# Optimization experiments

Measured on AMD Instinct MI355X. Metric: run time of the kernel, lower is better.

Reference implementation:

```python
import jax, jax.numpy as jnp
import numpy as np

L, N, D, E, KD = 4, 40000, 128, 320000, 16
DECAY, N_ITER, EPS = 0.5, 3, 1e-5


def setup_inputs() -> dict:
    key = jax.random.key(0)
    ks = jax.random.split(key, 16)
    s = 0.05
    return {
        "x": jax.random.normal(ks[0], (L, N, D), jnp.float32),
        "edge_rows": jax.random.randint(ks[1], (E,), 0, N, jnp.int32),
        "edge_cols": jax.random.randint(ks[2], (E,), 0, N, jnp.int32),
        "edge_vals": jax.random.uniform(ks[3], (E,), jnp.float32) * 0.1,
        "sage_W": jax.random.normal(ks[4], (D, D), jnp.float32) * s,
        "sage_b": jnp.zeros((D,), jnp.float32),
        "sage_agg_W": jax.random.normal(ks[5], (D, D), jnp.float32) * s,
        "key_W": jax.random.normal(ks[6], (D, KD), jnp.float32) * s,
        "query_W": jax.random.normal(ks[7], (D, KD), jnp.float32) * s,
        "value_W": jax.random.normal(ks[8], (D, D), jnp.float32) * s,
        "attn_ln_g": jnp.ones((D,), jnp.float32),
        "attn_ln_b": jnp.zeros((D,), jnp.float32),
        "lin_W": jax.random.normal(ks[9], (D, D), jnp.float32) * s,
        "lin_b": jnp.zeros((D,), jnp.float32),
        "ln_g": jnp.ones((D,), jnp.float32),
        "ln_b": jnp.zeros((D,), jnp.float32),
    }


def _layernorm(x, g, b):
    mu = jnp.mean(x, axis=-1, keepdims=True)
    var = jnp.mean((x - mu) ** 2, axis=-1, keepdims=True)
    return (x - mu) * jax.lax.rsqrt(var + EPS) * g + b


def _spmm(rows, cols, vals, x2d):
    # sparse [N,N] @ dense [N,F]: out[r] = sum_e vals[e] * x2d[cols[e]] for rows[e]==r
    return jax.ops.segment_sum(vals[:, None] * x2d[cols], rows, num_segments=N)


def reference(x, edge_rows, edge_cols, edge_vals, sage_W, sage_b, sage_agg_W,
              key_W, query_W, value_W, attn_ln_g, attn_ln_b,
              lin_W, lin_b, ln_g, ln_b):
    # x: [L, N, D]
    x2d = jnp.transpose(x, (1, 0, 2)).reshape(N, L * D)  # [N, L*D]

    # ---- SAGEConv ----
    proj = x @ sage_W + sage_b
    agg = _spmm(edge_rows, edge_cols, edge_vals, x2d)
    agg = jnp.transpose(agg.reshape(N, L, D), (1, 0, 2)) @ sage_agg_W
    sage_out = jax.nn.silu(proj + agg)

    # ---- RetentiveAttention ----
    weights = jnp.mean((x @ key_W) * (x @ query_W), axis=-1, keepdims=True)
    x_acc = x
    cur = x2d
    for _ in range(1, N_ITER):
        cur = _spmm(edge_rows, edge_cols, edge_vals, cur * DECAY)
        xr = jnp.transpose(cur.reshape(N, L, D), (1, 0, 2))  # [L, N, D]
        weights = weights + jnp.mean((xr @ key_W) * (xr @ query_W), axis=-1, keepdims=True)
        x_acc = x_acc + xr
    attn_out = _layernorm((x_acc @ value_W) * weights, attn_ln_g, attn_ln_b)

    # ---- GPSConv fusion ----
    y = jax.nn.silu((sage_out + attn_out) @ lin_W + lin_b)
    return _layernorm(y, ln_g, ln_b)
```

## Files before the change

### kernel.cpp

```cpp
#include <hip/hip_runtime.h>
#include <math.h>

#define LL 4
#define NN 40000
#define DD 128
#define EE 320000
#define ROWS (LL*NN)
#define ND (NN*DD)
#define EPS_LN 1e-5f

typedef __attribute__((ext_vector_type(8))) short bf16x8;
typedef __attribute__((ext_vector_type(4))) short s16x4;
typedef __attribute__((ext_vector_type(4))) float f32x4;

#define OFF_CNT      0
#define OFF_ROWPTR   40000
#define OFF_ROWOFS   80004
#define OFF_CCOLS    120004
#define OFF_CVALS    440004
#define OFF_WBF      760004
#define OFF_A        829636
#define OFF_B        (OFF_A + ROWS*DD/2)
#define OFF_XBF      (OFF_B + ROWS*DD/2)

#define WB_W0  0
#define WB_W1  32768
#define WB_WV  65536
#define WB_WL  98304
#define WB_K   131072
#define WB_Q   135168
#define WB_LO_BIG 16384
#define WB_LO_KQ  2048
#define WB_LOGICAL 69632

__device__ __forceinline__ unsigned fu(float f) { union { float f; unsigned u; } v; v.f = f; return v.u; }
__device__ __forceinline__ float uf(unsigned u) { union { unsigned u; float f; } v; v.u = u; return v.f; }

__device__ __forceinline__ short f2bf(float f) {
    unsigned u = fu(f);
    unsigned r = u + 0x7fffu + ((u >> 16) & 1u);
    return (short)(r >> 16);
}
__device__ __forceinline__ float bf2f(short h) { return uf(((unsigned)(unsigned short)h) << 16); }
__device__ __forceinline__ void splitbf(float v, short& h, short& l) {
    h = f2bf(v);
    l = f2bf(v - bf2f(h));
}

__device__ __forceinline__ unsigned pack_hi(float a, float b) {
    return (fu(a) >> 16) | (fu(b) & 0xffff0000u);
}
__device__ __forceinline__ float resid(float a) {
    return a - uf(fu(a) & 0xffff0000u);
}

union FragU { bf16x8 v; unsigned u[4]; };

__global__ void k_hist(const int* __restrict__ rows, int* __restrict__ cnt) {
    int e = blockIdx.x * 256 + threadIdx.x;
    if (e < EE) atomicAdd(&cnt[rows[e]], 1);
}

__global__ __launch_bounds__(1024) void k_scan1(const int* __restrict__ cnt,
                                                int* __restrict__ row_ptr,
                                                int* __restrict__ bsum) {
    __shared__ int wtot[16];
    int tid = threadIdx.x, lane = tid & 63, wid = tid >> 6;
    int i = blockIdx.x * 1024 + tid;
    int v = (i < NN) ? cnt[i] : 0;
    int incl = v;
    #pragma unroll
    for (int off = 1; off < 64; off <<= 1) {
        int t = __shfl_up(incl, off);
        if (lane >= off) incl += t;
    }
    if (lane == 63) wtot[wid] = incl;
    __syncthreads();
    if (wid == 0) {
        int wv = (lane < 16) ? wtot[lane] : 0;
        #pragma unroll
        for (int off = 1; off < 16; off <<= 1) {
            int t = __shfl_up(wv, off);
            if (lane >= off) wv += t;
        }
        if (lane < 16) wtot[lane] = wv;
    }
    __syncthreads();
    int excl = ((wid > 0) ? wtot[wid - 1] : 0) + incl - v;
    if (i < NN) row_ptr[i] = excl;
    if (tid == 0) bsum[blockIdx.x] = wtot[15];
}

__global__ void k_scan2(const int* __restrict__ bsum, int* __restrict__ bofs) {
    int lane = threadIdx.x;
    int v = (lane < 40) ? bsum[lane] : 0;
    int incl = v;
    #pragma unroll
    for (int off = 1; off < 64; off <<= 1) {
        int t = __shfl_up(incl, off);
        if (lane >= off) incl += t;
    }
    if (lane < 40) bofs[lane] = incl - v;
    if (lane == 39) bofs[40] = incl;
}

__global__ __launch_bounds__(1024) void k_scan3(const int* __restrict__ bofs,
                                                int* __restrict__ row_ptr,
                                                int* __restrict__ row_ofs) {
    int i = blockIdx.x * 1024 + threadIdx.x;
    int add = bofs[blockIdx.x];
    if (i < NN) {
        int v = row_ptr[i] + add;
        row_ptr[i] = v;
        row_ofs[i] = v;
    }
    if (i == NN) row_ptr[NN] = bofs[40];
}

__global__ void k_scatter(const int* __restrict__ rows, const int* __restrict__ cols,
                          const float* __restrict__ vals, int* __restrict__ row_ofs,
                          int* __restrict__ csr_cols, float* __restrict__ csr_vals) {
    int e = blockIdx.x * 256 + threadIdx.x;
    if (e < EE) {
        int r = rows[e];
        int p = atomicAdd(&row_ofs[r], 1);
        csr_cols[p] = cols[e];
        csr_vals[p] = vals[e];
    }
}

__global__ __launch_bounds__(256) void k_xcast(const float* __restrict__ x, short* __restrict__ o) {
    int t = blockIdx.x * 256 + threadIdx.x;
    int n = t >> 4;
    int d8 = (t & 15) * 8;
    #pragma unroll
    for (int l = 0; l < LL; ++l) {
        const float* xp = x + (size_t)l * ND + (size_t)n * 128 + d8;
        f32x4 a = *(const f32x4*)xp;
        f32x4 b = *(const f32x4*)(xp + 4);
        bf16x8 r;
        #pragma unroll
        for (int j = 0; j < 4; ++j) { r[j] = f2bf(a[j]); r[j + 4] = f2bf(b[j]); }
        *(bf16x8*)(o + (size_t)n * 512 + l * 128 + d8) = r;
    }
}

__global__ __launch_bounds__(256) void k_spmm(const short* __restrict__ in,
                                              const int* __restrict__ row_ptr,
                                              const int* __restrict__ ccols,
                                              const float* __restrict__ cvals,
                                              short* __restrict__ out) {
    int r = blockIdx.x * 4 + (threadIdx.x >> 6);
    int lane = threadIdx.x & 63;
    const short* inl = in + lane * 8;
    float acc[8] = {0.f, 0.f, 0.f, 0.f, 0.f, 0.f, 0.f, 0.f};
    int e0 = row_ptr[r], e1 = row_ptr[r + 1];
    int e = e0;
    for (; e + 8 <= e1; e += 8) {
        int cc[8]; float vv[8]; bf16x8 xv[8];
        #pragma unroll
        for (int j = 0; j < 8; ++j) { cc[j] = ccols[e + j]; vv[j] = cvals[e + j]; }
        #pragma unroll
        for (int j = 0; j < 8; ++j) xv[j] = *(const bf16x8*)(inl + (size_t)cc[j] * 512);
        #pragma unroll
        for (int j = 0; j < 8; ++j)
            #pragma unroll
            for (int k = 0; k < 8; ++k) acc[k] += vv[j] * bf2f(xv[j][k]);
    }
    for (; e + 4 <= e1; e += 4) {
        int cc[4]; float vv[4]; bf16x8 xv[4];
        #pragma unroll
        for (int j = 0; j < 4; ++j) { cc[j] = ccols[e + j]; vv[j] = cvals[e + j]; }
        #pragma unroll
        for (int j = 0; j < 4; ++j) xv[j] = *(const bf16x8*)(inl + (size_t)cc[j] * 512);
        #pragma unroll
        for (int j = 0; j < 4; ++j)
            #pragma unroll
            for (int k = 0; k < 8; ++k) acc[k] += vv[j] * bf2f(xv[j][k]);
    }
    for (; e < e1; ++e) {
        int c = ccols[e];
        float v = cvals[e];
        bf16x8 xv = *(const bf16x8*)(inl + (size_t)c * 512);
        #pragma unroll
        for (int k = 0; k < 8; ++k) acc[k] += v * bf2f(xv[k]);
    }
    bf16x8 o;
    #pragma unroll
    for (int k = 0; k < 8; ++k) o[k] = f2bf(acc[k]);
    *(bf16x8*)(out + (size_t)r * 512 + lane * 8) = o;
}

__global__ void k_prep(const float* __restrict__ W0, const float* __restrict__ W1,
                       const float* __restrict__ Wv, const float* __restrict__ Wl,
                       const float* __restrict__ Kw, const float* __restrict__ Qw,
                       short* __restrict__ o) {
    int t = blockIdx.x * 256 + threadIdx.x;
    if (t >= WB_LOGICAL) return;
    float v;
    int hi_idx, lo_idx;
    if (t < 65536) {
        int m = t >> 14, idx = t & 16383;
        int nn = idx >> 7, kk = idx & 127;
        const float* M = (m == 0) ? W0 : (m == 1) ? W1 : (m == 2) ? Wv : Wl;
        v = M[kk * 128 + nn];
        hi_idx = m * 32768 + idx;
        lo_idx = hi_idx + WB_LO_BIG;
    } else {
        int t2 = t - 65536;
        int sel = t2 >> 11;
        int idx = t2 & 2047;
        int nn = idx >> 7, kk = idx & 127;
        const float* M = sel ? Qw : Kw;
        v = M[kk * 16 + nn];
        hi_idx = WB_K + sel * 4096 + idx;
        lo_idx = hi_idx + WB_LO_KQ;
    }
    short h, l;
    splitbf(v, h, l);
    o[hi_idx] = h;
    o[lo_idx] = l;
}

#define MFMA(a, b, c) __builtin_amdgcn_mfma_f32_16x16x32_bf16(a, b, c, 0, 0, 0)

__global__ __launch_bounds__(256) void k_dense(
    const float* __restrict__ x, const short* __restrict__ A, const short* __restrict__ B,
    const short* __restrict__ wbf,
    const float* __restrict__ sage_b, const float* __restrict__ attn_g,
    const float* __restrict__ attn_b, const float* __restrict__ lin_b,
    const float* __restrict__ ln_g, const float* __restrict__ ln_b,
    float* __restrict__ out)
{
    __shared__ short pv[4][2][2048];
    const int tid = threadIdx.x;
    const int w = tid >> 6;
    const int lane = tid & 63;
    const int n = lane & 15;
    const int q = lane >> 4;
    const int rowA = blockIdx.x * 64 + w * 16 + n;
    const int l = rowA / NN;
    const int node = rowA - l * NN;
    char* pB = (char*)&pv[w][0][0];
    char* vB = (char*)&pv[w][1][0];

    bf16x8 xh[4], ah[4];
    f32x4 kx = {0,0,0,0}, qx = {0,0,0,0};
    f32x4 ka = {0,0,0,0}, qa = {0,0,0,0};
    f32x4 kb = {0,0,0,0}, qb = {0,0,0,0};

    {
        const float* xp = x + (size_t)rowA * 128 + q * 8;
        const short* ap = A + (size_t)node * 512 + l * 128 + q * 8;
        const short* bp = B + (size_t)node * 512 + l * 128 + q * 8;
        const short* Kp = wbf + WB_K + n * 128 + q * 8;
        const short* Qp = wbf + WB_Q + n * 128 + q * 8;
        #pragma unroll
        for (int s = 0; s < 4; ++s) {
            f32x4 x0 = *(const f32x4*)(xp + s * 32);
            f32x4 x1 = *(const f32x4*)(xp + s * 32 + 4);
            bf16x8 av = *(const bf16x8*)(ap + s * 32);
            bf16x8 bv = *(const bf16x8*)(bp + s * 32);

            f32x4 c0, c1;
            #pragma unroll
            for (int j = 0; j < 4; ++j) {
                c0[j] = x0[j] + 0.5f * bf2f(av[j])     + 0.25f * bf2f(bv[j]);
                c1[j] = x1[j] + 0.5f * bf2f(av[j + 4]) + 0.25f * bf2f(bv[j + 4]);
            }

            FragU fxh, fxl, fch;
            #pragma unroll
            for (int i = 0; i < 2; ++i) {
                fxh.u[i]     = pack_hi(x0[2*i], x0[2*i+1]);
                fxh.u[i + 2] = pack_hi(x1[2*i], x1[2*i+1]);
                fxl.u[i]     = pack_hi(resid(x0[2*i]), resid(x0[2*i+1]));
                fxl.u[i + 2] = pack_hi(resid(x1[2*i]), resid(x1[2*i+1]));
                fch.u[i]     = pack_hi(c0[2*i], c0[2*i+1]);
                fch.u[i + 2] = pack_hi(c1[2*i], c1[2*i+1]);
            }
            xh[s] = fxh.v; ah[s] = av;
            int cbyte = (n * 256 + s * 64 + q * 16) ^ ((n & 7) << 4);
            *(bf16x8*)(vB + cbyte) = fch.v;

            bf16x8 bkh = *(const bf16x8*)(Kp + s * 32);
            bf16x8 bkl = *(const bf16x8*)(Kp + WB_LO_KQ + s * 32);
            bf16x8 bqh = *(const bf16x8*)(Qp + s * 32);
            bf16x8 bql = *(const bf16x8*)(Qp + WB_LO_KQ + s * 32);
            kx = MFMA(fxh.v, bkh, kx); kx = MFMA(fxl.v, bkh, kx); kx = MFMA(fxh.v, bkl, kx);
            qx = MFMA(fxh.v, bqh, qx); qx = MFMA(fxl.v, bqh, qx); qx = MFMA(fxh.v, bql, qx);
            ka = MFMA(av, bkh, ka); qa = MFMA(av, bqh, qa);
            kb = MFMA(bv, bkh, kb); qb = MFMA(bv, bqh, qb);
        }
    }
    asm volatile("" ::: "memory");

    f32x4 wts;
    #pragma unroll
    for (int r = 0; r < 4; ++r) {
        float p = kx[r] * qx[r] + 0.25f * (ka[r] * qa[r]) + 0.0625f * (kb[r] * qb[r]);
        p += __shfl_xor(p, 1);
        p += __shfl_xor(p, 2);
        p += __shfl_xor(p, 4);
        p += __shfl_xor(p, 8);
        wts[r] = p * (1.f / 16.f);
    }

    {
        f32x4 S[8];
        #pragma unroll
        for (int t = 0; t < 8; ++t) {
            float bv = sage_b[t * 16 + n];
            S[t] = (f32x4){bv, bv, bv, bv};
        }
        #pragma unroll
        for (int s = 0; s < 4; ++s) {
            #pragma unroll
            for (int t = 0; t < 8; ++t) {
                bf16x8 w0h = *(const bf16x8*)(wbf + WB_W0 + (t * 16 + n) * 128 + s * 32 + q * 8);
                S[t] = MFMA(xh[s], w0h, S[t]);
                bf16x8 w1h = *(const bf16x8*)(wbf + WB_W1 + (t * 16 + n) * 128 + s * 32 + q * 8);
                S[t] = MFMA(ah[s], w1h, S[t]);
            }
        }
        #pragma unroll
        for (int t = 0; t < 8; ++t)
            #pragma unroll
            for (int r = 0; r < 4; ++r) {
                float v = S[t][r];
                v = v / (1.f + __expf(-v));
                int row = q * 4 + r;
                int byte = (row * 256 + (t * 16 + n) * 2) ^ ((row & 7) << 4);
                *(short*)(pB + byte) = f2bf(v);
            }
    }
    asm volatile("" ::: "memory");

    float mu_n, rs_n;
    {
        f32x4 V[8];
        #pragma unroll
        for (int t = 0; t < 8; ++t) V[t] = (f32x4){0.f, 0.f, 0.f, 0.f};
        #pragma unroll
        for (int s = 0; s < 4; ++s) {
            int cbyte = (n * 256 + s * 64 + q * 16) ^ ((n & 7) << 4);
            bf16x8 chs = *(const bf16x8*)(vB + cbyte);
            #pragma unroll
            for (int t = 0; t < 8; ++t) {
                bf16x8 wvh = *(const bf16x8*)(wbf + WB_WV + (t * 16 + n) * 128 + s * 32 + q * 8);
                V[t] = MFMA(chs, wvh, V[t]);
            }
        }
        f32x4 s1 = {0,0,0,0}, s2 = {0,0,0,0};
        #pragma unroll
        for (int t = 0; t < 8; ++t)
            #pragma unroll
            for (int r = 0; r < 4; ++r) {
                float v = V[t][r] * wts[r];
                V[t][r] = v;
                s1[r] += v; s2[r] += v * v;
            }
        #pragma unroll
        for (int r = 0; r < 4; ++r) {
            float a1 = s1[r], a2 = s2[r];
            a1 += __shfl_xor(a1, 1); a2 += __shfl_xor(a2, 1);
            a1 += __shfl_xor(a1, 2); a2 += __shfl_xor(a2, 2);
            a1 += __shfl_xor(a1, 4); a2 += __shfl_xor(a2, 4);
            a1 += __shfl_xor(a1, 8); a2 += __shfl_xor(a2, 8);
            s1[r] = a1; s2[r] = a2;
        }
        float mu4[4], rs4[4];
        #pragma unroll
        for (int r = 0; r < 4; ++r) {
            mu4[r] = s1[r] * (1.f / 128.f);
            float var = s2[r] * (1.f / 128.f) - mu4[r] * mu4[r];
            rs4[r] = rsqrtf(var + EPS_LN);
        }
        #pragma unroll
        for (int t = 0; t < 8; ++t)
            #pragma unroll
            for (int r = 0; r < 4; ++r) {
                int row = q * 4 + r;
                int byte = (row * 256 + (t * 16 + n) * 2) ^ ((row & 7) << 4);
                *(short*)(vB + byte) = f2bf(V[t][r]);
            }
        int src = (n >> 2) << 4;
        float mA = __shfl(mu4[0], src), mB_ = __shfl(mu4[1], src);
        float mC = __shfl(mu4[2], src), mD = __shfl(mu4[3], src);
        float rA = __shfl(rs4[0], src), rB_ = __shfl(rs4[1], src);
        float rC = __shfl(rs4[2], src), rD = __shfl(rs4[3], src);
        float m01 = (n & 1) ? mB_ : mA, m23 = (n & 1) ? mD : mC;
        float r01 = (n & 1) ? rB_ : rA, r23 = (n & 1) ? rD : rC;
        mu_n = (n & 2) ? m23 : m01;
        rs_n = (n & 2) ? r23 : r01;
    }
    asm volatile("" ::: "memory");

    bf16x8 zh[4];
    #pragma unroll
    for (int s = 0; s < 4; ++s) {
        int byte = (n * 256 + s * 64 + q * 16) ^ ((n & 7) << 4);
        bf16x8 ph = *(const bf16x8*)(pB + byte);
        bf16x8 vh = *(const bf16x8*)(vB + byte);
        const float* gp = attn_g + s * 32 + q * 8;
        const float* bp = attn_b + s * 32 + q * 8;
        f32x4 g0 = *(const f32x4*)gp, g1 = *(const f32x4*)(gp + 4);
        f32x4 b0 = *(const f32x4*)bp, b1 = *(const f32x4*)(bp + 4);
        float z[8];
        #pragma unroll
        for (int j = 0; j < 4; ++j) {
            z[j]     = bf2f(ph[j])     + (bf2f(vh[j])     - mu_n) * rs_n * g0[j] + b0[j];
            z[j + 4] = bf2f(ph[j + 4]) + (bf2f(vh[j + 4]) - mu_n) * rs_n * g1[j] + b1[j];
        }
        FragU f;
        f.u[0] = pack_hi(z[0], z[1]); f.u[1] = pack_hi(z[2], z[3]);
        f.u[2] = pack_hi(z[4], z[5]); f.u[3] = pack_hi(z[6], z[7]);
        zh[s] = f.v;
    }
    f32x4 F[8];
    #pragma unroll
    for (int t = 0; t < 8; ++t) {
        float bv = lin_b[t * 16 + n];
        F[t] = (f32x4){bv, bv, bv, bv};
    }
    #pragma unroll
    for (int s = 0; s < 4; ++s)
        #pragma unroll
        for (int t = 0; t < 8; ++t) {
            bf16x8 wlh = *(const bf16x8*)(wbf + WB_WL + (t * 16 + n) * 128 + s * 32 + q * 8);
            F[t] = MFMA(zh[s], wlh, F[t]);
        }
    f32x4 t1 = {0,0,0,0}, t2 = {0,0,0,0};
    #pragma unroll
    for (int t = 0; t < 8; ++t)
        #pragma unroll
        for (int r = 0; r < 4; ++r) {
            float v = F[t][r];
            v = v / (1.f + __expf(-v));
            F[t][r] = v;
            t1[r] += v; t2[r] += v * v;
        }
    #pragma unroll
    for (int r = 0; r < 4; ++r) {
        float a1 = t1[r], a2 = t2[r];
        a1 += __shfl_xor(a1, 1); a2 += __shfl_xor(a2, 1);
        a1 += __shfl_xor(a1, 2); a2 += __shfl_xor(a2, 2);
        a1 += __shfl_xor(a1, 4); a2 += __shfl_xor(a2, 4);
        a1 += __shfl_xor(a1, 8); a2 += __shfl_xor(a2, 8);
        t1[r] = a1; t2[r] = a2;
    }
    #pragma unroll
    for (int t = 0; t < 8; ++t) {
        float g = ln_g[t * 16 + n];
        float bb = ln_b[t * 16 + n];
        #pragma unroll
        for (int r = 0; r < 4; ++r) {
            float mu = t1[r] * (1.f / 128.f);
            float var = t2[r] * (1.f / 128.f) - mu * mu;
            float rs = rsqrtf(var + EPS_LN);
            size_t row = (size_t)blockIdx.x * 64 + w * 16 + q * 4 + r;
            out[row * 128 + t * 16 + n] = (F[t][r] - mu) * rs * g + bb;
        }
    }
}

extern "C" void kernel_launch(void* const* d_in, const int* in_sizes, int n_in,
                              void* d_out, int out_size, void* d_ws, size_t ws_size,
                              hipStream_t stream) {
    const float* x       = (const float*)d_in[0];
    const int*   erows   = (const int*)d_in[1];
    const int*   ecols   = (const int*)d_in[2];
    const float* evals   = (const float*)d_in[3];
    const float* sage_W  = (const float*)d_in[4];
    const float* sage_b  = (const float*)d_in[5];
    const float* sage_aW = (const float*)d_in[6];
    const float* key_W   = (const float*)d_in[7];
    const float* query_W = (const float*)d_in[8];
    const float* value_W = (const float*)d_in[9];
    const float* attn_g  = (const float*)d_in[10];
    const float* attn_b  = (const float*)d_in[11];
    const float* lin_W   = (const float*)d_in[12];
    const float* lin_b   = (const float*)d_in[13];
    const float* ln_g    = (const float*)d_in[14];
    const float* ln_b    = (const float*)d_in[15];
    float* out = (float*)d_out;

    int*   wsi = (int*)d_ws;
    float* wsf = (float*)d_ws;
    int*   cnt      = wsi + OFF_CNT;
    int*   row_ptr  = wsi + OFF_ROWPTR;
    int*   row_ofs  = wsi + OFF_ROWOFS;
    int*   csr_cols = wsi + OFF_CCOLS;
    float* csr_vals = wsf + OFF_CVALS;
    short* wbf      = (short*)(wsf + OFF_WBF);
    short* Abf      = (short*)(wsf + OFF_A);
    short* Bbf      = (short*)(wsf + OFF_B);
    short* Xbf      = (short*)(wsf + OFF_XBF);
    int*   bsum     = (int*)(wsf + OFF_A);
    int*   bofs     = bsum + 64;

    hipMemsetAsync(cnt, 0, NN * sizeof(int), stream);
    k_hist<<<(EE + 255) / 256, 256, 0, stream>>>(erows, cnt);
    k_prep<<<(WB_LOGICAL + 255) / 256, 256, 0, stream>>>(sage_W, sage_aW, value_W, lin_W,
                                                         key_W, query_W, wbf);
    k_xcast<<<NN * 16 / 256, 256, 0, stream>>>(x, Xbf);
    k_scan1<<<40, 1024, 0, stream>>>(cnt, row_ptr, bsum);
    k_scan2<<<1, 64, 0, stream>>>(bsum, bofs);
    k_scan3<<<40, 1024, 0, stream>>>(bofs, row_ptr, row_ofs);
    k_scatter<<<(EE + 255) / 256, 256, 0, stream>>>(erows, ecols, evals, row_ofs, csr_cols, csr_vals);

    k_spmm<<<NN / 4, 256, 0, stream>>>(Xbf, row_ptr, csr_cols, csr_vals, Abf);
    k_spmm<<<NN / 4, 256, 0, stream>>>(Abf, row_ptr, csr_cols, csr_vals, Bbf);

    k_dense<<<ROWS / 64, 256, 0, stream>>>(x, Abf, Bbf, wbf, sage_b, attn_g, attn_b,
                                           lin_b, ln_g, ln_b, out);
}
```

Baseline: 530.0 us.

## Process two CSR rows per wave in SpMM and halve dense-kernel accumulator live ranges

The SpMM kernel now has each wavefront handle two consecutive rows, interleaving their gathers so more independent loads are in flight, and the grid is halved to match. In the dense kernel the 8-tile accumulator arrays for the SAGE, value and linear GEMMs are split into two half passes of 4 tiles. The combined C fragments stay in registers instead of going through LDS. The final SiLU output is staged through LDS as float before the layernorm. The aim is to lower register pressure for better occupancy and more memory-level parallelism, at the cost of extra LDS traffic, fewer SpMM waves and some imbalance between paired rows.

```diff
diff --git a/kernel.cpp b/kernel.cpp
--- a/kernel.cpp
+++ b/kernel.cpp
@@ -150,45 +150,63 @@
                                               const int* __restrict__ ccols,
                                               const float* __restrict__ cvals,
                                               short* __restrict__ out) {
-    int r = blockIdx.x * 4 + (threadIdx.x >> 6);
+    int wid = blockIdx.x * 4 + (threadIdx.x >> 6);
+    int rA = wid * 2;
     int lane = threadIdx.x & 63;
     const short* inl = in + lane * 8;
-    float acc[8] = {0.f, 0.f, 0.f, 0.f, 0.f, 0.f, 0.f, 0.f};
-    int e0 = row_ptr[r], e1 = row_ptr[r + 1];
-    int e = e0;
-    for (; e + 8 <= e1; e += 8) {
-        int cc[8]; float vv[8]; bf16x8 xv[8];
-        #pragma unroll
-        for (int j = 0; j < 8; ++j) { cc[j] = ccols[e + j]; vv[j] = cvals[e + j]; }
-        #pragma unroll
-        for (int j = 0; j < 8; ++j) xv[j] = *(const bf16x8*)(inl + (size_t)cc[j] * 512);
-        #pragma unroll
-        for (int j = 0; j < 8; ++j)
-            #pragma unroll
-            for (int k = 0; k < 8; ++k) acc[k] += vv[j] * bf2f(xv[j][k]);
-    }
-    for (; e + 4 <= e1; e += 4) {
-        int cc[4]; float vv[4]; bf16x8 xv[4];
-        #pragma unroll
-        for (int j = 0; j < 4; ++j) { cc[j] = ccols[e + j]; vv[j] = cvals[e + j]; }
-        #pragma unroll
-        for (int j = 0; j < 4; ++j) xv[j] = *(const bf16x8*)(inl + (size_t)cc[j] * 512);
+    float accA[8] = {0.f,0.f,0.f,0.f,0.f,0.f,0.f,0.f};
+    float accB[8] = {0.f,0.f,0.f,0.f,0.f,0.f,0.f,0.f};
+    int a0 = row_ptr[rA], a1 = row_ptr[rA + 1], b1 = row_ptr[rA + 2];
+    int b0 = a1;
+    while (a0 + 4 <= a1 && b0 + 4 <= b1) {
+        int ca[4], cb[4]; float va[4], vb[4]; bf16x8 xa[4], xb[4];
+        #pragma unroll
+        for (int j = 0; j < 4; ++j) {
+            ca[j] = ccols[a0 + j]; va[j] = cvals[a0 + j];
+            cb[j] = ccols[b0 + j]; vb[j] = cvals[b0 + j];
+        }
+        #pragma unroll
+        for (int j = 0; j < 4; ++j) {
+            xa[j] = *(const bf16x8*)(inl + (size_t)ca[j] * 512);
+            xb[j] = *(const bf16x8*)(inl + (size_t)cb[j] * 512);
+        }
         #pragma unroll
         for (int j = 0; j < 4; ++j)
             #pragma unroll
-            for (int k = 0; k < 8; ++k) acc[k] += vv[j] * bf2f(xv[j][k]);
-    }
-    for (; e < e1; ++e) {
-        int c = ccols[e];
-        float v = cvals[e];
-        bf16x8 xv = *(const bf16x8*)(inl + (size_t)c * 512);
-        #pragma unroll
-        for (int k = 0; k < 8; ++k) acc[k] += v * bf2f(xv[k]);
-    }
-    bf16x8 o;
-    #pragma unroll
-    for (int k = 0; k < 8; ++k) o[k] = f2bf(acc[k]);
-    *(bf16x8*)(out + (size_t)r * 512 + lane * 8) = o;
+            for (int k = 0; k < 8; ++k) {
+                accA[k] += va[j] * bf2f(xa[j][k]);
+                accB[k] += vb[j] * bf2f(xb[j][k]);
+            }
+        a0 += 4; b0 += 4;
+    }
+    #pragma unroll 1
+    for (int pass = 0; pass < 2; ++pass) {
+        int e = pass ? b0 : a0, e1 = pass ? b1 : a1;
+        float* acc = pass ? accB : accA;
+        for (; e + 4 <= e1; e += 4) {
+            int cc[4]; float vv[4]; bf16x8 xv[4];
+            #pragma unroll
+            for (int j = 0; j < 4; ++j) { cc[j] = ccols[e + j]; vv[j] = cvals[e + j]; }
+            #pragma unroll
+            for (int j = 0; j < 4; ++j) xv[j] = *(const bf16x8*)(inl + (size_t)cc[j] * 512);
+            #pragma unroll
+            for (int j = 0; j < 4; ++j)
+                #pragma unroll
+                for (int k = 0; k < 8; ++k) acc[k] += vv[j] * bf2f(xv[j][k]);
+        }
+        for (; e < e1; ++e) {
+            int c = ccols[e];
+            float v = cvals[e];
+            bf16x8 xv = *(const bf16x8*)(inl + (size_t)c * 512);
+            #pragma unroll
+            for (int k = 0; k < 8; ++k) acc[k] += v * bf2f(xv[k]);
+        }
+    }
+    bf16x8 oA, oB;
+    #pragma unroll
+    for (int k = 0; k < 8; ++k) { oA[k] = f2bf(accA[k]); oB[k] = f2bf(accB[k]); }
+    *(bf16x8*)(out + (size_t)rA * 512 + lane * 8) = oA;
+    *(bf16x8*)(out + (size_t)(rA + 1) * 512 + lane * 8) = oB;
 }
 
 __global__ void k_prep(const float* __restrict__ W0, const float* __restrict__ W1,
@@ -244,7 +262,7 @@
     char* pB = (char*)&pv[w][0][0];
     char* vB = (char*)&pv[w][1][0];
 
-    bf16x8 xh[4], ah[4];
+    bf16x8 xh[4], ah[4], ch[4];
     f32x4 kx = {0,0,0,0}, qx = {0,0,0,0};
     f32x4 ka = {0,0,0,0}, qa = {0,0,0,0};
     f32x4 kb = {0,0,0,0}, qb = {0,0,0,0};
@@ -279,9 +297,7 @@
                 fch.u[i]     = pack_hi(c0[2*i], c0[2*i+1]);
                 fch.u[i + 2] = pack_hi(c1[2*i], c1[2*i+1]);
             }
-            xh[s] = fxh.v; ah[s] = av;
-            int cbyte = (n * 256 + s * 64 + q * 16) ^ ((n & 7) << 4);
-            *(bf16x8*)(vB + cbyte) = fch.v;
+            xh[s] = fxh.v; ah[s] = av; ch[s] = fch.v;
 
             bf16x8 bkh = *(const bf16x8*)(Kp + s * 32);
             bf16x8 bkl = *(const bf16x8*)(Kp + WB_LO_KQ + s * 32);
@@ -293,7 +309,6 @@
             kb = MFMA(bv, bkh, kb); qb = MFMA(bv, bqh, qb);
         }
     }
-    asm volatile("" ::: "memory");
 
     f32x4 wts;
     #pragma unroll
@@ -306,31 +321,33 @@
         wts[r] = p * (1.f / 16.f);
     }
 
-    {
-        f32x4 S[8];
-        #pragma unroll
-        for (int t = 0; t < 8; ++t) {
-            float bv = sage_b[t * 16 + n];
+    #pragma unroll 1
+    for (int h = 0; h < 2; ++h) {
+        f32x4 S[4];
+        #pragma unroll
+        for (int t = 0; t < 4; ++t) {
+            float bv = sage_b[(h * 4 + t) * 16 + n];
             S[t] = (f32x4){bv, bv, bv, bv};
         }
         #pragma unroll
         for (int s = 0; s < 4; ++s) {
             #pragma unroll
-            for (int t = 0; t < 8; ++t) {
-                bf16x8 w0h = *(const bf16x8*)(wbf + WB_W0 + (t * 16 + n) * 128 + s * 32 + q * 8);
+            for (int t = 0; t < 4; ++t) {
+                int col = (h * 4 + t) * 16 + n;
+                bf16x8 w0h = *(const bf16x8*)(wbf + WB_W0 + col * 128 + s * 32 + q * 8);
                 S[t] = MFMA(xh[s], w0h, S[t]);
-                bf16x8 w1h = *(const bf16x8*)(wbf + WB_W1 + (t * 16 + n) * 128 + s * 32 + q * 8);
+                bf16x8 w1h = *(const bf16x8*)(wbf + WB_W1 + col * 128 + s * 32 + q * 8);
                 S[t] = MFMA(ah[s], w1h, S[t]);
             }
         }
         #pragma unroll
-        for (int t = 0; t < 8; ++t)
+        for (int t = 0; t < 4; ++t)
             #pragma unroll
             for (int r = 0; r < 4; ++r) {
                 float v = S[t][r];
                 v = v / (1.f + __expf(-v));
                 int row = q * 4 + r;
-                int byte = (row * 256 + (t * 16 + n) * 2) ^ ((row & 7) << 4);
+                int byte = (row * 256 + ((h * 4 + t) * 16 + n) * 2) ^ ((row & 7) << 4);
                 *(short*)(pB + byte) = f2bf(v);
             }
     }
@@ -338,28 +355,31 @@
 
     float mu_n, rs_n;
     {
-        f32x4 V[8];
-        #pragma unroll
-        for (int t = 0; t < 8; ++t) V[t] = (f32x4){0.f, 0.f, 0.f, 0.f};
-        #pragma unroll
-        for (int s = 0; s < 4; ++s) {
-            int cbyte = (n * 256 + s * 64 + q * 16) ^ ((n & 7) << 4);
-            bf16x8 chs = *(const bf16x8*)(vB + cbyte);
-            #pragma unroll
-            for (int t = 0; t < 8; ++t) {
-                bf16x8 wvh = *(const bf16x8*)(wbf + WB_WV + (t * 16 + n) * 128 + s * 32 + q * 8);
-                V[t] = MFMA(chs, wvh, V[t]);
-            }
-        }
         f32x4 s1 = {0,0,0,0}, s2 = {0,0,0,0};
-        #pragma unroll
-        for (int t = 0; t < 8; ++t)
-            #pragma unroll
-            for (int r = 0; r < 4; ++r) {
-                float v = V[t][r] * wts[r];
-                V[t][r] = v;
-                s1[r] += v; s2[r] += v * v;
-            }
+        #pragma unroll 1
+        for (int h = 0; h < 2; ++h) {
+            f32x4 V[4];
+            #pragma unroll
+            for (int t = 0; t < 4; ++t) V[t] = (f32x4){0.f, 0.f, 0.f, 0.f};
+            #pragma unroll
+            for (int s = 0; s < 4; ++s)
+                #pragma unroll
+                for (int t = 0; t < 4; ++t) {
+                    int col = (h * 4 + t) * 16 + n;
+                    bf16x8 wvh = *(const bf16x8*)(wbf + WB_WV + col * 128 + s * 32 + q * 8);
+                    V[t] = MFMA(ch[s], wvh, V[t]);
+                }
+            #pragma unroll
+            for (int t = 0; t < 4; ++t)
+                #pragma unroll
+                for (int r = 0; r < 4; ++r) {
+                    float v = V[t][r] * wts[r];
+                    s1[r] += v; s2[r] += v * v;
+                    int row = q * 4 + r;
+                    int byte = (row * 256 + ((h * 4 + t) * 16 + n) * 2) ^ ((row & 7) << 4);
+                    *(short*)(vB + byte) = f2bf(v);
+                }
+        }
         #pragma unroll
         for (int r = 0; r < 4; ++r) {
             float a1 = s1[r], a2 = s2[r];
@@ -376,14 +396,6 @@
             float var = s2[r] * (1.f / 128.f) - mu4[r] * mu4[r];
             rs4[r] = rsqrtf(var + EPS_LN);
         }
-        #pragma unroll
-        for (int t = 0; t < 8; ++t)
-            #pragma unroll
-            for (int r = 0; r < 4; ++r) {
-                int row = q * 4 + r;
-                int byte = (row * 256 + (t * 16 + n) * 2) ^ ((row & 7) << 4);
-                *(short*)(vB + byte) = f2bf(V[t][r]);
-            }
         int src = (n >> 2) << 4;
         float mA = __shfl(mu4[0], src), mB_ = __shfl(mu4[1], src);
         float mC = __shfl(mu4[2], src), mD = __shfl(mu4[3], src);
@@ -417,29 +429,37 @@
         f.u[2] = pack_hi(z[4], z[5]); f.u[3] = pack_hi(z[6], z[7]);
         zh[s] = f.v;
     }
-    f32x4 F[8];
-    #pragma unroll
-    for (int t = 0; t < 8; ++t) {
-        float bv = lin_b[t * 16 + n];
-        F[t] = (f32x4){bv, bv, bv, bv};
-    }
-    #pragma unroll
-    for (int s = 0; s < 4; ++s)
-        #pragma unroll
-        for (int t = 0; t < 8; ++t) {
-            bf16x8 wlh = *(const bf16x8*)(wbf + WB_WL + (t * 16 + n) * 128 + s * 32 + q * 8);
-            F[t] = MFMA(zh[s], wlh, F[t]);
-        }
+    asm volatile("" ::: "memory");
+
+    float* fz = (float*)pB;
     f32x4 t1 = {0,0,0,0}, t2 = {0,0,0,0};
-    #pragma unroll
-    for (int t = 0; t < 8; ++t)
-        #pragma unroll
-        for (int r = 0; r < 4; ++r) {
-            float v = F[t][r];
-            v = v / (1.f + __expf(-v));
-            F[t][r] = v;
-            t1[r] += v; t2[r] += v * v;
-        }
+    #pragma unroll 1
+    for (int h = 0; h < 2; ++h) {
+        f32x4 F[4];
+        #pragma unroll
+        for (int t = 0; t < 4; ++t) {
+            float bv = lin_b[(h * 4 + t) * 16 + n];
+            F[t] = (f32x4){bv, bv, bv, bv};
+        }
+        #pragma unroll
+        for (int s = 0; s < 4; ++s)
+            #pragma unroll
+            for (int t = 0; t < 4; ++t) {
+                int col = (h * 4 + t) * 16 + n;
+                bf16x8 wlh = *(const bf16x8*)(wbf + WB_WL + col * 128 + s * 32 + q * 8);
+                F[t] = MFMA(zh[s], wlh, F[t]);
+            }
+        #pragma unroll
+        for (int t = 0; t < 4; ++t)
+            #pragma unroll
+            for (int r = 0; r < 4; ++r) {
+                float v = F[t][r];
+                v = v / (1.f + __expf(-v));
+                t1[r] += v; t2[r] += v * v;
+                fz[(q * 4 + r) * 128 + (h * 4 + t) * 16 + n] = v;
+            }
+    }
+    asm volatile("" ::: "memory");
     #pragma unroll
     for (int r = 0; r < 4; ++r) {
         float a1 = t1[r], a2 = t2[r];
@@ -458,8 +478,9 @@
             float mu = t1[r] * (1.f / 128.f);
             float var = t2[r] * (1.f / 128.f) - mu * mu;
             float rs = rsqrtf(var + EPS_LN);
+            float v = fz[(q * 4 + r) * 128 + t * 16 + n];
             size_t row = (size_t)blockIdx.x * 64 + w * 16 + q * 4 + r;
-            out[row * 128 + t * 16 + n] = (F[t][r] - mu) * rs * g + bb;
+            out[row * 128 + t * 16 + n] = (v - mu) * rs * g + bb;
         }
     }
 }
@@ -509,8 +530,8 @@
     k_scan3<<<40, 1024, 0, stream>>>(bofs, row_ptr, row_ofs);
     k_scatter<<<(EE + 255) / 256, 256, 0, stream>>>(erows, ecols, evals, row_ofs, csr_cols, csr_vals);
 
-    k_spmm<<<NN / 4, 256, 0, stream>>>(Xbf, row_ptr, csr_cols, csr_vals, Abf);
-    k_spmm<<<NN / 4, 256, 0, stream>>>(Abf, row_ptr, csr_cols, csr_vals, Bbf);
+    k_spmm<<<NN / 8, 256, 0, stream>>>(Xbf, row_ptr, csr_cols, csr_vals, Abf);
+    k_spmm<<<NN / 8, 256, 0, stream>>>(Abf, row_ptr, csr_cols, csr_vals, Bbf);
 
     k_dense<<<ROWS / 64, 256, 0, stream>>>(x, Abf, Bbf, wbf, sage_b, attn_g, attn_b,
                                            lin_b, ln_g, ln_b, out);
```

New measurement: 550.0 us. 3.8% more time.
